# Kernel tuning notes

Measured on AMD Instinct MI355X. Metric: run time of the kernel, lower is better.

## Reference

```python
import jax, jax.numpy as jnp
import numpy as np

COUPLING = 1.0
DT = 1.0
ATTRACTION = 1.0
EPS = 1e-6


def setup_inputs() -> dict:
    key = jax.random.key(0)
    k1, k2, k3, k4 = jax.random.split(key, 4)
    B, N, D = 4, 2048, 4
    theta_prev = jax.random.normal(k1, (B, N, D), dtype=jnp.float32)
    gamma_prev = jax.random.normal(k2, (B, N, D), dtype=jnp.float32)
    theta_connectivity_weight = jax.random.uniform(k3, (B, N, N), dtype=jnp.float32)
    alpha_t = jax.random.normal(k4, (B, N, N), dtype=jnp.float32)
    return {
        "theta_prev": theta_prev,
        "gamma_prev": gamma_prev,
        "theta_connectivity_weight": theta_connectivity_weight,
        "alpha_t": alpha_t,
    }


def reference(theta_prev, gamma_prev, theta_connectivity_weight, alpha_t):
    # Pairwise coupling: coupling/N * sum_j W[b,i,j] * sin(theta[b,j,d] - theta[b,i,d] - alpha[b,i,j])
    # Expanded via trig identities so the O(N^2*D) tensor is never materialized:
    #   sin(tj - ti - a) = cos(a)*(s_j c_i - c_j s_i) - sin(a)*(c_j c_i + s_j s_i)
    # => sum_j W_ij sin(...) = c_i*(A s)_i - s_i*(A c)_i - c_i*(Bm c)_i - s_i*(Bm s)_i
    # with A = W*cos(alpha), Bm = W*sin(alpha). This matches the chunked torch loop exactly.
    n = theta_prev.shape[1]
    s = jnp.sin(theta_prev)  # [B, N, D]
    c = jnp.cos(theta_prev)  # [B, N, D]
    A = theta_connectivity_weight * jnp.cos(alpha_t)   # [B, N, N]
    Bm = theta_connectivity_weight * jnp.sin(alpha_t)  # [B, N, N]
    As = jnp.einsum("bij,bjd->bid", A, s)
    Ac = jnp.einsum("bij,bjd->bid", A, c)
    Bs = jnp.einsum("bij,bjd->bid", Bm, s)
    Bc = jnp.einsum("bij,bjd->bid", Bm, c)
    coupling_term = (COUPLING / n) * (c * As - s * Ac - c * Bc - s * Bs)
    drive_term = ATTRACTION * (gamma_prev - theta_prev)
    theta_next = theta_prev + DT * (drive_term + coupling_term)
    # torch F.normalize: x / clamp(||x||_2, min=eps) along last dim
    norm = jnp.linalg.norm(theta_next, axis=-1, keepdims=True)
    return theta_next / jnp.maximum(norm, EPS)
```

## Files before the change

### kernel.cpp

```cpp
#include <hip/hip_runtime.h>
#include <stdint.h>

#define N_NODES 2048
#define N_BATCH 4
#define ROWS_PER_BLOCK 8
#define THREADS 512

__device__ __forceinline__ uint32_t bf16rn(float x) {
    uint32_t u = __float_as_uint(x);
    u += 0x7fffu + ((u >> 16) & 1u);
    return u >> 16;
}

__global__ __launch_bounds__(THREADS, 2) void kuramoto_kernel(
    const float* __restrict__ theta,
    const float* __restrict__ gamma,
    const float* __restrict__ W,
    const float* __restrict__ alpha,
    float* __restrict__ out)
{
    __shared__ uint4 table[N_NODES];
    __shared__ float red[ROWS_PER_BLOCK * 16 * 64];

    const int tid  = threadIdx.x;
    const int lane = tid & 63;
    const int wave = tid >> 6;
    const int b    = blockIdx.x >> 8;
    const int i    = ((blockIdx.x & 255) * ROWS_PER_BLOCK) + wave;

    const float* thb = theta + (size_t)b * (N_NODES * 4);
    #pragma unroll
    for (int g = 0; g < N_NODES / THREADS; ++g) {
        const int j = tid + g * THREADS;
        const float4 u = *(const float4*)(thb + (size_t)j * 4);
        const float th[4] = {u.x, u.y, u.z, u.w};
        uint32_t p[4];
        #pragma unroll
        for (int d = 0; d < 4; ++d) {
            float s, c;
            __sincosf(th[d], &s, &c);
            p[d] = (bf16rn(c) << 16) | bf16rn(s);
        }
        table[j] = make_uint4(p[0], p[1], p[2], p[3]);
    }
    __syncthreads();

    const size_t rowbase = ((size_t)b * N_NODES + i) * N_NODES;
    const float* Wr = W + rowbase;
    const float* Ar = alpha + rowbase;

    float aAs[4] = {0.f, 0.f, 0.f, 0.f};
    float aAc[4] = {0.f, 0.f, 0.f, 0.f};
    float aBs[4] = {0.f, 0.f, 0.f, 0.f};
    float aBc[4] = {0.f, 0.f, 0.f, 0.f};

    #pragma unroll 8
    for (int it = 0; it < N_NODES / 64; ++it) {
        const int j = it * 64 + lane;
        const float w = Wr[j];
        const float a = Ar[j];
        float sa, ca;
        __sincosf(a, &sa, &ca);
        const float A  = w * ca;
        const float Bq = w * sa;
        const uint4 t = table[j];
        const uint32_t tw[4] = {t.x, t.y, t.z, t.w};
        #pragma unroll
        for (int d = 0; d < 4; ++d) {
            const float s = __uint_as_float(tw[d] << 16);
            const float c = __uint_as_float(tw[d] & 0xffff0000u);
            aAs[d] = fmaf(A,  s, aAs[d]);
            aAc[d] = fmaf(A,  c, aAc[d]);
            aBs[d] = fmaf(Bq, s, aBs[d]);
            aBc[d] = fmaf(Bq, c, aBc[d]);
        }
    }

    float* myred = red + wave * (16 * 64);
    #pragma unroll
    for (int d = 0; d < 4; ++d) {
        myred[(0 * 4 + d) * 64 + (lane ^ (0 * 4 + d))] = aAs[d];
        myred[(1 * 4 + d) * 64 + (lane ^ (1 * 4 + d))] = aAc[d];
        myred[(2 * 4 + d) * 64 + (lane ^ (2 * 4 + d))] = aBs[d];
        myred[(3 * 4 + d) * 64 + (lane ^ (3 * 4 + d))] = aBc[d];
    }
    __syncthreads();

    const int v   = lane & 15;
    const int seg = lane >> 4;
    float sum = 0.0f;
    #pragma unroll
    for (int m = 0; m < 16; ++m)
        sum += myred[v * 64 + ((seg * 16 + m) ^ v)];
    sum += __shfl_xor(sum, 16, 64);
    sum += __shfl_xor(sum, 32, 64);

    const int d = lane & 3;
    const float As = __shfl(sum,      d, 64);
    const float Ac = __shfl(sum,  4 + d, 64);
    const float Bs = __shfl(sum,  8 + d, 64);
    const float Bc = __shfl(sum, 12 + d, 64);

    if (lane < 4) {
        const float th_i = thb[(size_t)i * 4 + d];
        float s_i, c_i;
        __sincosf(th_i, &s_i, &c_i);
        const float coup = (c_i * As - s_i * Ac - c_i * Bc - s_i * Bs)
                           * (1.0f / (float)N_NODES);
        const size_t oidx = ((size_t)b * N_NODES + i) * 4 + d;
        const float g = gamma[oidx];
        const float t = g + coup;
        float s2 = t * t;
        s2 += __shfl_xor(s2, 1, 64);
        s2 += __shfl_xor(s2, 2, 64);
        const float nrm = sqrtf(s2);
        const float inv = 1.0f / fmaxf(nrm, 1e-6f);
        out[oidx] = t * inv;
    }
}

extern "C" void kernel_launch(void* const* d_in, const int* in_sizes, int n_in,
                              void* d_out, int out_size, void* d_ws, size_t ws_size,
                              hipStream_t stream) {
    const float* theta = (const float*)d_in[0];
    const float* gamma = (const float*)d_in[1];
    const float* W     = (const float*)d_in[2];
    const float* alpha = (const float*)d_in[3];
    float* out = (float*)d_out;

    const int grid = (N_BATCH * N_NODES) / ROWS_PER_BLOCK;
    hipLaunchKernelGGL(kuramoto_kernel, dim3(grid), dim3(THREADS), 0, stream,
                       theta, gamma, W, alpha, out);
}
```

Measured before the change: 153.1 us.

## Merge accumulators into complex re/im sums and reduce via wave shuffles

```diff
diff --git a/kernel.cpp b/kernel.cpp
--- a/kernel.cpp
+++ b/kernel.cpp
@@ -12,7 +12,7 @@
     return u >> 16;
 }
 
-__global__ __launch_bounds__(THREADS, 2) void kuramoto_kernel(
+__global__ __launch_bounds__(THREADS, 8) void kuramoto_kernel(
     const float* __restrict__ theta,
     const float* __restrict__ gamma,
     const float* __restrict__ W,
@@ -20,7 +20,6 @@
     float* __restrict__ out)
 {
     __shared__ uint4 table[N_NODES];
-    __shared__ float red[ROWS_PER_BLOCK * 16 * 64];
 
     const int tid  = threadIdx.x;
     const int lane = tid & 63;
@@ -49,10 +48,8 @@
     const float* Wr = W + rowbase;
     const float* Ar = alpha + rowbase;
 
-    float aAs[4] = {0.f, 0.f, 0.f, 0.f};
-    float aAc[4] = {0.f, 0.f, 0.f, 0.f};
-    float aBs[4] = {0.f, 0.f, 0.f, 0.f};
-    float aBc[4] = {0.f, 0.f, 0.f, 0.f};
+    float re[4] = {0.f, 0.f, 0.f, 0.f};
+    float im[4] = {0.f, 0.f, 0.f, 0.f};
 
     #pragma unroll 8
     for (int it = 0; it < N_NODES / 64; ++it) {
@@ -69,53 +66,40 @@
         for (int d = 0; d < 4; ++d) {
             const float s = __uint_as_float(tw[d] << 16);
             const float c = __uint_as_float(tw[d] & 0xffff0000u);
-            aAs[d] = fmaf(A,  s, aAs[d]);
-            aAc[d] = fmaf(A,  c, aAc[d]);
-            aBs[d] = fmaf(Bq, s, aBs[d]);
-            aBc[d] = fmaf(Bq, c, aBc[d]);
+            re[d] = fmaf(A,  c, re[d]);
+            re[d] = fmaf(Bq, s, re[d]);
+            im[d] = fmaf(A,  s, im[d]);
+            im[d] = fmaf(-Bq, c, im[d]);
         }
     }
 
-    float* myred = red + wave * (16 * 64);
     #pragma unroll
-    for (int d = 0; d < 4; ++d) {
-        myred[(0 * 4 + d) * 64 + (lane ^ (0 * 4 + d))] = aAs[d];
-        myred[(1 * 4 + d) * 64 + (lane ^ (1 * 4 + d))] = aAc[d];
-        myred[(2 * 4 + d) * 64 + (lane ^ (2 * 4 + d))] = aBs[d];
-        myred[(3 * 4 + d) * 64 + (lane ^ (3 * 4 + d))] = aBc[d];
+    for (int stage = 1; stage < 64; stage <<= 1) {
+        #pragma unroll
+        for (int d = 0; d < 4; ++d) {
+            re[d] += __shfl_xor(re[d], stage, 64);
+            im[d] += __shfl_xor(im[d], stage, 64);
+        }
     }
-    __syncthreads();
 
-    const int v   = lane & 15;
-    const int seg = lane >> 4;
-    float sum = 0.0f;
-    #pragma unroll
-    for (int m = 0; m < 16; ++m)
-        sum += myred[v * 64 + ((seg * 16 + m) ^ v)];
-    sum += __shfl_xor(sum, 16, 64);
-    sum += __shfl_xor(sum, 32, 64);
-
-    const int d = lane & 3;
-    const float As = __shfl(sum,      d, 64);
-    const float Ac = __shfl(sum,  4 + d, 64);
-    const float Bs = __shfl(sum,  8 + d, 64);
-    const float Bc = __shfl(sum, 12 + d, 64);
-
-    if (lane < 4) {
-        const float th_i = thb[(size_t)i * 4 + d];
-        float s_i, c_i;
-        __sincosf(th_i, &s_i, &c_i);
-        const float coup = (c_i * As - s_i * Ac - c_i * Bc - s_i * Bs)
-                           * (1.0f / (float)N_NODES);
-        const size_t oidx = ((size_t)b * N_NODES + i) * 4 + d;
-        const float g = gamma[oidx];
-        const float t = g + coup;
-        float s2 = t * t;
-        s2 += __shfl_xor(s2, 1, 64);
-        s2 += __shfl_xor(s2, 2, 64);
-        const float nrm = sqrtf(s2);
-        const float inv = 1.0f / fmaxf(nrm, 1e-6f);
-        out[oidx] = t * inv;
+    if (lane == 0) {
+        const size_t obase = ((size_t)b * N_NODES + i) * 4;
+        const float4 th4 = *(const float4*)(thb + (size_t)i * 4);
+        const float4 g4  = *(const float4*)(gamma + obase);
+        const float thd[4] = {th4.x, th4.y, th4.z, th4.w};
+        const float gd[4]  = {g4.x, g4.y, g4.z, g4.w};
+        float t[4];
+        float s2 = 0.0f;
+        #pragma unroll
+        for (int d = 0; d < 4; ++d) {
+            float s_i, c_i;
+            __sincosf(thd[d], &s_i, &c_i);
+            const float coup = (c_i * im[d] - s_i * re[d]) * (1.0f / (float)N_NODES);
+            t[d] = gd[d] + coup;
+            s2 = fmaf(t[d], t[d], s2);
+        }
+        const float inv = 1.0f / fmaxf(sqrtf(s2), 1e-6f);
+        *(float4*)(out + obase) = make_float4(t[0]*inv, t[1]*inv, t[2]*inv, t[3]*inv);
     }
 }
 
```

Result: no change. 152.4 us (-0.5%).
